# Performance work log

Measured on AMD Instinct MI355X. Metric: run time of the kernel, lower is better.

Reference implementation:

```python
import jax, jax.numpy as jnp
import numpy as np

BG_CLASS = 3          # eval path drops argmax-class==3
NMS_THRESH = 0.2      # nms(rois, scores, 0.2)
IMG_SIZE = 512.0      # ClipBoxes to 512x512 image
NUM_CLASSES = 4


def _decode_boxes(rois, deltas):
    # BBoxTransform: std weights (0.1, 0.1, 0.2, 0.2), then clip to image
    w = rois[:, 2] - rois[:, 0]
    h = rois[:, 3] - rois[:, 1]
    cx = rois[:, 0] + 0.5 * w
    cy = rois[:, 1] + 0.5 * h
    dx = deltas[:, 0] * 0.1
    dy = deltas[:, 1] * 0.1
    dw = deltas[:, 2] * 0.2
    dh = deltas[:, 3] * 0.2
    pcx = cx + dx * w
    pcy = cy + dy * h
    pw = jnp.exp(dw) * w
    ph = jnp.exp(dh) * h
    boxes = jnp.stack([pcx - 0.5 * pw, pcy - 0.5 * ph,
                       pcx + 0.5 * pw, pcy + 0.5 * ph], axis=1)
    return jnp.clip(boxes, 0.0, IMG_SIZE)


def _iou_one_vs_all(box, boxes):
    x1 = jnp.maximum(box[0], boxes[:, 0])
    y1 = jnp.maximum(box[1], boxes[:, 1])
    x2 = jnp.minimum(box[2], boxes[:, 2])
    y2 = jnp.minimum(box[3], boxes[:, 3])
    inter = jnp.clip(x2 - x1, 0.0) * jnp.clip(y2 - y1, 0.0)
    area_a = (box[2] - box[0]) * (box[3] - box[1])
    area_b = (boxes[:, 2] - boxes[:, 0]) * (boxes[:, 3] - boxes[:, 1])
    return inter / (area_a + area_b - inter + 1e-8)


def _nms_keep_mask(boxes, scores, thresh):
    # Fixed-shape NMS: returns bool keep mask over the original ordering.
    N = boxes.shape[0]
    order = jnp.argsort(-scores)           # descending score
    b = boxes[order]
    idx = jnp.arange(N)

    def body(i, keep):
        iou = _iou_one_vs_all(b[i], b)
        suppress = (iou > thresh) & (idx > i)
        return jnp.where(keep[i], keep & ~suppress, keep)

    keep_sorted = jax.lax.fori_loop(0, N, body, jnp.ones((N,), dtype=bool))
    return jnp.zeros((N,), dtype=bool).at[order].set(keep_sorted)


def _head(f, rois, w6, b6, w7, b7, wc, bc, wr, br):
    # TwoMLPHead
    v = jax.nn.relu(f @ w6.T + b6)          # [N, 1024]
    v = jax.nn.relu(v @ w7.T + b7)          # [N, 1024]
    # FastRCNNPredictor
    c = v @ wc.T + bc                        # [N, num_classes]
    r = v @ wr.T + br                        # [N, num_classes*4]
    classes = jnp.argmax(c, axis=1)          # torch.max(x,1)[1]
    scores = jnp.max(c, axis=1)              # torch.max(x,1)[0]
    deltas = jnp.take_along_axis(r.reshape(-1, NUM_CLASSES, 4),
                                 classes[:, None, None], axis=1)[:, 0, :]
    boxes = _decode_boxes(rois, deltas)
    return scores, classes, boxes


def setup_inputs() -> dict:
    key = jax.random.key(0)
    ks = jax.random.split(key, 10)
    N, D, H = 8000, 12544, 1024
    f = jax.random.normal(ks[0], (N, D), dtype=jnp.float32)
    # valid xyxy ROIs inside 512x512
    xy = jax.random.uniform(ks[1], (N, 2), minval=0.0, maxval=380.0)
    wh = jax.random.uniform(ks[2], (N, 2), minval=20.0, maxval=120.0)
    rois = jnp.concatenate([xy, xy + wh], axis=1).astype(jnp.float32)
    w6 = jax.random.normal(ks[3], (H, D), dtype=jnp.float32) * 0.01
    b6 = jnp.zeros((H,), dtype=jnp.float32)
    w7 = jax.random.normal(ks[4], (H, H), dtype=jnp.float32) * 0.02
    b7 = jnp.zeros((H,), dtype=jnp.float32)
    wc = jax.random.normal(ks[5], (NUM_CLASSES, H), dtype=jnp.float32) * 0.02
    bc = jnp.zeros((NUM_CLASSES,), dtype=jnp.float32)
    wr = jax.random.normal(ks[6], (NUM_CLASSES * 4, H), dtype=jnp.float32) * 0.02
    br = jnp.zeros((NUM_CLASSES * 4,), dtype=jnp.float32)
    return {"f": f, "rois": rois, "w6": w6, "b6": b6, "w7": w7, "b7": b7,
            "wc": wc, "bc": bc, "wr": wr, "br": br}


def reference(f, rois, w6, b6, w7, b7, wc, bc, wr, br):
    scores, classes, boxes = _head(f, rois, w6, b6, w7, b7, wc, bc, wr, br)
    valid = classes != BG_CLASS
    s_masked = jnp.where(valid, scores, -jnp.inf)
    keep = _nms_keep_mask(boxes, s_masked, NMS_THRESH) & valid
    # fixed-shape equivalent of (scores[index], labels[index], bboxes[index])
    return scores, classes, boxes, keep
```

## Files before the change

### kernel.cpp

```cpp
#include <hip/hip_runtime.h>
#include <hip/hip_fp16.h>
#include <math.h>

typedef _Float16 f16;
typedef _Float16 f16x4 __attribute__((ext_vector_type(4)));
typedef _Float16 f16x8 __attribute__((ext_vector_type(8)));
typedef float f32x4 __attribute__((ext_vector_type(4)));
typedef unsigned long long u64;

#define GLD16(g, s) __builtin_amdgcn_global_load_lds( \
    (const __attribute__((address_space(1))) void*)(g), \
    (__attribute__((address_space(3))) void*)(s), 16, 0, 0)

struct HL { f16 h, l; };
__device__ __forceinline__ HL split1(float e) {
  float em = __uint_as_float(__float_as_uint(e) & 0xFFFFE000u);
  HL r;
  r.h = (f16)em;
  r.l = (f16)(e - em);
  return r;
}

__global__ __launch_bounds__(256) void split_kernel(const float* __restrict__ src,
                                                    f16* __restrict__ hi,
                                                    f16* __restrict__ lo,
                                                    long n4, float scale) {
  long stride = (long)gridDim.x * blockDim.x;
  for (long i = (long)blockIdx.x * blockDim.x + threadIdx.x; i < n4; i += stride) {
    float4 v = ((const float4*)src)[i];
    f16x4 h, l;
    HL r0 = split1(v.x * scale); h[0] = r0.h; l[0] = r0.l;
    HL r1 = split1(v.y * scale); h[1] = r1.h; l[1] = r1.l;
    HL r2 = split1(v.z * scale); h[2] = r2.h; l[2] = r2.l;
    HL r3 = split1(v.w * scale); h[3] = r3.h; l[3] = r3.l;
    ((f16x4*)hi)[i] = h;
    ((f16x4*)lo)[i] = l;
  }
}

template<int EPI, int AFP32>
__global__ __launch_bounds__(512) void gemm_split(
    const void* __restrict__ Av1, const void* __restrict__ Av2,
    const f16* __restrict__ B1, const f16* __restrict__ B2,
    const float* __restrict__ bias,
    void* __restrict__ out1, void* __restrict__ out2,
    const int M, const int K) {
  __shared__ __align__(16) char smem[3][49152];
  const int tid = threadIdx.x;
  const int lane = tid & 63;
  const int wid = tid >> 6;
  const int wr = wid >> 1, wcol = wid & 1;
  const int m0 = blockIdx.y * 256;
  const int n0 = blockIdx.x * 128;

  f32x4 acc[4][4];
#pragma unroll
  for (int m = 0; m < 4; ++m)
#pragma unroll
    for (int n = 0; n < 4; ++n) acc[m][n] = (f32x4){0.f, 0.f, 0.f, 0.f};

  const int cg = (((tid & 3) ^ ((tid >> 3) & 3)) * 8);
  const f16* gB1 = B1 + (size_t)(n0 + (tid >> 2)) * K + cg;
  const f16* gB2 = B2 + (size_t)(n0 + (tid >> 2)) * K + cg;

  const float* gAf[4];
  if (AFP32) {
    const float* Af = (const float*)Av1;
#pragma unroll
    for (int q = 0; q < 4; ++q) {
      int rowg = m0 + q * 64 + (tid >> 3);
      if (rowg > M - 1) rowg = M - 1;
      const int chunkg = (tid & 7) ^ ((tid >> 3) & 7);
      gAf[q] = Af + (size_t)rowg * K + chunkg * 4;
    }
  }
  const f16 *gA1q0 = nullptr, *gA1q1 = nullptr, *gA2q0 = nullptr, *gA2q1 = nullptr;
  if (!AFP32) {
    int ra0 = m0 + (tid >> 2);       if (ra0 > M - 1) ra0 = M - 1;
    int ra1 = m0 + 128 + (tid >> 2); if (ra1 > M - 1) ra1 = M - 1;
    gA1q0 = (const f16*)Av1 + (size_t)ra0 * K + cg;
    gA1q1 = (const f16*)Av1 + (size_t)ra1 * K + cg;
    gA2q0 = (const f16*)Av2 + (size_t)ra0 * K + cg;
    gA2q1 = (const f16*)Av2 + (size_t)ra1 * K + cg;
  }

  const int arow = wr * 64 + (lane & 15);
  const int brow = wcol * 64 + (lane & 15);
  const int kcA = (((lane >> 4) ^ ((arow >> 1) & 3)) * 8);
  const int kcB = (((lane >> 4) ^ ((brow >> 1) & 3)) * 8);
  const int pA0 = (((lane >> 4) * 2)     ^ (arow & 7)) * 4;
  const int pA1 = (((lane >> 4) * 2 + 1) ^ (arow & 7)) * 4;

  const int nt = K / 32;

#define STAGE(buf, kt)                                            \
  do {                                                            \
    char* smx_ = smem[buf];                                       \
    if (AFP32) {                                                  \
      float* db = (float*)smx_;                                   \
      GLD16(gAf[0] + (kt), db + 0 * 2048 + wid * 256);            \
      GLD16(gAf[1] + (kt), db + 1 * 2048 + wid * 256);            \
      GLD16(gAf[2] + (kt), db + 2 * 2048 + wid * 256);            \
      GLD16(gAf[3] + (kt), db + 3 * 2048 + wid * 256);            \
    } else {                                                      \
      f16* d1 = (f16*)smx_;                                       \
      f16* d2 = d1 + 8192;                                        \
      GLD16(gA1q0 + (kt), d1 + wid * 512);                        \
      GLD16(gA1q1 + (kt), d1 + 4096 + wid * 512);                 \
      GLD16(gA2q0 + (kt), d2 + wid * 512);                        \
      GLD16(gA2q1 + (kt), d2 + 4096 + wid * 512);                 \
    }                                                             \
    GLD16(gB1 + (kt), (f16*)(smx_ + 32768) + wid * 512);          \
    GLD16(gB2 + (kt), (f16*)(smx_ + 40960) + wid * 512);          \
  } while (0)

  STAGE(0, 0);
  if (nt > 1) STAGE(1, 32);
  int cur = 0;

  for (int t = 0; t < nt; ++t) {
    if (t + 1 < nt) asm volatile("s_waitcnt vmcnt(6)" ::: "memory");
    else            asm volatile("s_waitcnt vmcnt(0)" ::: "memory");
    asm volatile("s_waitcnt lgkmcnt(0)" ::: "memory");
    __builtin_amdgcn_s_barrier();
    __builtin_amdgcn_sched_barrier(0);

    const char* smx = smem[cur];
    f16x8 a1[4], a2[4], b1[4], b2[4];
    if (AFP32) {
      const float* sf = (const float*)smx;
#pragma unroll
      for (int m = 0; m < 4; ++m) {
        const float* rp = sf + (arow + m * 16) * 32;
        f32x4 u = *(const f32x4*)(rp + pA0);
        f32x4 v = *(const f32x4*)(rp + pA1);
        f16x8 h, l;
#pragma unroll
        for (int j = 0; j < 4; ++j) { HL r = split1(u[j] * 256.0f); h[j] = r.h; l[j] = r.l; }
#pragma unroll
        for (int j = 0; j < 4; ++j) { HL r = split1(v[j] * 256.0f); h[4 + j] = r.h; l[4 + j] = r.l; }
        a1[m] = h; a2[m] = l;
      }
    } else {
      const f16* s1 = (const f16*)smx;
      const f16* s2 = s1 + 8192;
#pragma unroll
      for (int m = 0; m < 4; ++m) {
        a1[m] = *(const f16x8*)&s1[(arow + m * 16) * 32 + kcA];
        a2[m] = *(const f16x8*)&s2[(arow + m * 16) * 32 + kcA];
      }
    }
    {
      const f16* sb1 = (const f16*)(smx + 32768);
      const f16* sb2 = (const f16*)(smx + 40960);
#pragma unroll
      for (int n = 0; n < 4; ++n) {
        b1[n] = *(const f16x8*)&sb1[(brow + n * 16) * 32 + kcB];
        b2[n] = *(const f16x8*)&sb2[(brow + n * 16) * 32 + kcB];
      }
    }

    int pre = cur + 2; if (pre >= 3) pre -= 3;
    if (t + 2 < nt) STAGE(pre, (t + 2) * 32);

#pragma unroll
    for (int m = 0; m < 4; ++m)
#pragma unroll
      for (int n = 0; n < 4; ++n)
        acc[m][n] = __builtin_amdgcn_mfma_f32_16x16x32_f16(a1[m], b1[n], acc[m][n], 0, 0, 0);
#pragma unroll
    for (int m = 0; m < 4; ++m)
#pragma unroll
      for (int n = 0; n < 4; ++n)
        acc[m][n] = __builtin_amdgcn_mfma_f32_16x16x32_f16(a2[m], b1[n], acc[m][n], 0, 0, 0);
#pragma unroll
    for (int m = 0; m < 4; ++m)
#pragma unroll
      for (int n = 0; n < 4; ++n)
        acc[m][n] = __builtin_amdgcn_mfma_f32_16x16x32_f16(a1[m], b2[n], acc[m][n], 0, 0, 0);

    ++cur; if (cur >= 3) cur = 0;
  }
#undef STAGE

  const int crow = m0 + wr * 64 + 4 * (lane >> 4);
  const int ccol0 = n0 + wcol * 64 + (lane & 15);
#pragma unroll
  for (int n = 0; n < 4; ++n) {
    const int col = ccol0 + n * 16;
    const float bv = bias[col];
#pragma unroll
    for (int m = 0; m < 4; ++m) {
#pragma unroll
      for (int j = 0; j < 4; ++j) {
        const int row = crow + m * 16 + j;
        if (row < M) {
          float v = acc[m][n][j] * (1.0f / 65536.0f) + bv;
          v = fmaxf(v, 0.0f);
          if (EPI == 1) {
            HL r = split1(v * 256.0f);
            ((f16*)out1)[(size_t)row * 1024 + col] = r.h;
            ((f16*)out2)[(size_t)row * 1024 + col] = r.l;
          } else {
            ((float*)out1)[(size_t)row * 1024 + col] = v;
          }
        }
      }
    }
  }
}

__device__ __forceinline__ float dot4f(float4 a, float4 b) {
  return a.x * b.x + a.y * b.y + a.z * b.z + a.w * b.w;
}

__global__ __launch_bounds__(256) void head_final(
    const float* __restrict__ v7,
    const float* __restrict__ wc, const float* __restrict__ bc,
    const float* __restrict__ wr, const float* __restrict__ br,
    const float* __restrict__ rois,
    float* __restrict__ outScores, float* __restrict__ outClasses,
    float* __restrict__ outBoxes,
    float* __restrict__ smask, float* __restrict__ wsbox, int* __restrict__ wsval) {
  const int gw = (blockIdx.x * 256 + threadIdx.x) >> 6;
  const int lane = threadIdx.x & 63;
  if (gw >= 8000) return;

  const float4* vr = (const float4*)(v7 + (size_t)gw * 1024);
  float4 x0 = vr[lane], x1 = vr[64 + lane], x2 = vr[128 + lane], x3 = vr[192 + lane];

  float s[20];
#pragma unroll
  for (int o = 0; o < 20; ++o) {
    const float* wrow = (o < 4) ? (wc + o * 1024) : (wr + (o - 4) * 1024);
    const float4* w4 = (const float4*)wrow;
    float a = dot4f(x0, w4[lane]) + dot4f(x1, w4[64 + lane]) +
              dot4f(x2, w4[128 + lane]) + dot4f(x3, w4[192 + lane]);
#pragma unroll
    for (int off = 32; off >= 1; off >>= 1) a += __shfl_xor(a, off);
    s[o] = a + ((o < 4) ? bc[o] : br[o - 4]);
  }

  float best = s[0]; int cls = 0;
  if (s[1] > best) { best = s[1]; cls = 1; }
  if (s[2] > best) { best = s[2]; cls = 2; }
  if (s[3] > best) { best = s[3]; cls = 3; }

  float d0, d1, d2, d3;
  if      (cls == 0) { d0 = s[4];  d1 = s[5];  d2 = s[6];  d3 = s[7];  }
  else if (cls == 1) { d0 = s[8];  d1 = s[9];  d2 = s[10]; d3 = s[11]; }
  else if (cls == 2) { d0 = s[12]; d1 = s[13]; d2 = s[14]; d3 = s[15]; }
  else               { d0 = s[16]; d1 = s[17]; d2 = s[18]; d3 = s[19]; }

  float4 rb = ((const float4*)rois)[gw];
  float w = rb.z - rb.x, h = rb.w - rb.y;
  float cx = rb.x + 0.5f * w, cy = rb.y + 0.5f * h;
  float pcx = cx + d0 * 0.1f * w;
  float pcy = cy + d1 * 0.1f * h;
  float pw = expf(d2 * 0.2f) * w;
  float ph = expf(d3 * 0.2f) * h;
  float bx0 = fminf(fmaxf(pcx - 0.5f * pw, 0.f), 512.f);
  float by0 = fminf(fmaxf(pcy - 0.5f * ph, 0.f), 512.f);
  float bx1 = fminf(fmaxf(pcx + 0.5f * pw, 0.f), 512.f);
  float by1 = fminf(fmaxf(pcy + 0.5f * ph, 0.f), 512.f);

  if (lane == 0) {
    outScores[gw] = best;
    outClasses[gw] = (float)cls;
    outBoxes[gw * 4 + 0] = bx0;
    outBoxes[gw * 4 + 1] = by0;
    outBoxes[gw * 4 + 2] = bx1;
    outBoxes[gw * 4 + 3] = by1;
    int valid = (cls != 3);
    smask[gw] = valid ? best : -INFINITY;
    wsval[gw] = valid;
    float4 bb; bb.x = bx0; bb.y = by0; bb.z = bx1; bb.w = by1;
    ((float4*)wsbox)[gw] = bb;
  }
}

__global__ __launch_bounds__(256) void rank_kernel(
    const float* __restrict__ smask, const float* __restrict__ bx,
    const int* __restrict__ valid,
    int* __restrict__ order, float* __restrict__ sboxes, int* __restrict__ svalid) {
  __shared__ __align__(16) float sS[8000];
  const int tid = threadIdx.x;
  for (int i = tid; i < 8000; i += 256) sS[i] = smask[i];
  __syncthreads();
  const int i = blockIdx.x * 256 + tid;
  if (i >= 8000) return;
  const float si = sS[i];
  int cnt = 0;
  const float4* s4p = (const float4*)sS;
  for (int j4 = 0; j4 < 2000; ++j4) {
    float4 s4 = s4p[j4];
    int jb = j4 * 4;
    cnt += (s4.x > si) || (s4.x == si && (jb + 0) < i);
    cnt += (s4.y > si) || (s4.y == si && (jb + 1) < i);
    cnt += (s4.z > si) || (s4.z == si && (jb + 2) < i);
    cnt += (s4.w > si) || (s4.w == si && (jb + 3) < i);
  }
  order[cnt] = i;
  svalid[cnt] = valid[i];
  ((float4*)sboxes)[cnt] = ((const float4*)bx)[i];
}

__global__ __launch_bounds__(256) void iou_matrix(const float* __restrict__ sboxes,
                                                  u64* __restrict__ M,
                                                  u64* __restrict__ Mdiag,
                                                  const int* __restrict__ svalid) {
  const int t = blockIdx.y;
  const int w = blockIdx.x * 4 + (threadIdx.x >> 6);
  if (w < t || w >= 125) return;
  if (svalid[t * 64] == 0 || svalid[w * 64] == 0) return;
  const int lane = threadIdx.x & 63;
  const int ri = t * 64 + lane;
  float4 rb = ((const float4*)sboxes)[ri];
  const float ra = (rb.z - rb.x) * (rb.w - rb.y);
  const float4* cb = (const float4*)sboxes + w * 64;
  u64 bits = 0;
#pragma unroll 4
  for (int j = 0; j < 64; ++j) {
    float4 c = cb[j];
    float x1 = fmaxf(rb.x, c.x), y1 = fmaxf(rb.y, c.y);
    float x2 = fminf(rb.z, c.z), y2 = fminf(rb.w, c.w);
    float inter = fmaxf(x2 - x1, 0.f) * fmaxf(y2 - y1, 0.f);
    float ca = (c.z - c.x) * (c.w - c.y);
    float iou = inter / (ra + ca - inter + 1e-8f);
    int gc = w * 64 + j;
    if (iou > 0.2f && gc > ri) bits |= (1ULL << j);
  }
  M[(size_t)ri * 128 + w] = bits;
  if (w == t) Mdiag[(size_t)t * 64 + lane] = bits;
}

__global__ __launch_bounds__(128) void nms_scan(
    const u64* __restrict__ M, const u64* __restrict__ Mdiag,
    const int* __restrict__ order,
    const int* __restrict__ svalid, float* __restrict__ outKeep) {
  __shared__ __align__(16) u64 sMdiag[8000];
  __shared__ u64 acc[126];
  __shared__ unsigned char klist[64];
  __shared__ int kcount;
  __shared__ int tv[125];
  __shared__ int nvt_s;
  const int tid = threadIdx.x;
  for (int i = tid; i < 4000; i += 128)
    ((float4*)sMdiag)[i] = ((const float4*)Mdiag)[i];
  for (int w = tid; w < 125; w += 128) acc[w] = 0;
  if (tid < 125) tv[tid] = svalid[tid * 64];
  __syncthreads();
  if (tid == 0) {
    int c = 0;
    while (c < 125 && tv[c]) ++c;
    nvt_s = c;
  }
  __syncthreads();
  const int nvt = nvt_s;

  for (int t = 0; t < nvt; ++t) {
    if (tid < 64) {
      u64 myrow = sMdiag[t * 64 + tid];
      unsigned mlo = (unsigned)myrow, mhi = (unsigned)(myrow >> 32);
      u64 r = acc[t];
      u64 rem = ~r;
      while (rem) {
        int i = __builtin_ctzll(rem);
        unsigned rlo = (unsigned)__builtin_amdgcn_readlane((int)mlo, i);
        unsigned rhi = (unsigned)__builtin_amdgcn_readlane((int)mhi, i);
        u64 rowi = ((u64)rhi << 32) | (u64)rlo;
        r |= rowi;
        rem &= ~(rowi | (1ULL << i));
      }
      u64 kept = ~r;
      if (tid == 0) { acc[t] = r; kcount = (int)__popcll(kept); }
      if ((kept >> tid) & 1ULL)
        klist[__popcll(kept & ((1ULL << tid) - 1ULL))] = (unsigned char)tid;
    }
    __syncthreads();
    const int kc = kcount;
    const int w = t + 1 + tid;
    if (w < nvt) {
      u64 a = acc[w];
      const u64* base = M + (size_t)t * 64 * 128 + w;
      int j = 0;
      for (; j + 16 <= kc; j += 16) {
        u64 o = 0;
#pragma unroll
        for (int q = 0; q < 16; ++q) o |= base[(size_t)klist[j + q] * 128];
        a |= o;
      }
      for (; j + 4 <= kc; j += 4) {
        u64 v0 = base[(size_t)klist[j] * 128];
        u64 v1 = base[(size_t)klist[j + 1] * 128];
        u64 v2 = base[(size_t)klist[j + 2] * 128];
        u64 v3 = base[(size_t)klist[j + 3] * 128];
        a |= (v0 | v1) | (v2 | v3);
      }
      for (; j < kc; ++j) a |= base[(size_t)klist[j] * 128];
      acc[w] = a;
    }
    __syncthreads();
  }

  for (int p = tid; p < 8000; p += 128) {
    int removed = (int)((acc[p >> 6] >> (p & 63)) & 1ULL);
    float kv = (!removed && svalid[p]) ? 1.0f : 0.0f;
    outKeep[order[p]] = kv;
  }
}

extern "C" void kernel_launch(void* const* d_in, const int* in_sizes, int n_in,
                              void* d_out, int out_size, void* d_ws, size_t ws_size,
                              hipStream_t stream) {
  const float* F    = (const float*)d_in[0];
  const float* ROIS = (const float*)d_in[1];
  const float* W6   = (const float*)d_in[2];
  const float* B6   = (const float*)d_in[3];
  const float* W7   = (const float*)d_in[4];
  const float* B7   = (const float*)d_in[5];
  const float* WC   = (const float*)d_in[6];
  const float* BC   = (const float*)d_in[7];
  const float* WR   = (const float*)d_in[8];
  const float* BR   = (const float*)d_in[9];

  const size_t N = 8000, D = 12544, H = 1024;
  char* ws = (char*)d_ws;
  size_t off = 0;
  auto alloc = [&](size_t bytes) -> void* {
    void* p = (void*)(ws + off);
    off += (bytes + 255) & ~(size_t)255;
    return p;
  };
  f16*   B1w   = (f16*)alloc(H * D * 2);
  f16*   B2w   = (f16*)alloc(H * D * 2);
  f16*   V61   = (f16*)alloc(N * H * 2);
  f16*   V62   = (f16*)alloc(N * H * 2);
  f16*   W71   = (f16*)alloc(H * H * 2);
  f16*   W72   = (f16*)alloc(H * H * 2);
  float* V7    = (float*)alloc(N * H * 4);
  float* SMASK = (float*)alloc(N * 4);
  float* WSBOX = (float*)alloc(N * 16);
  int*   WSVAL = (int*)alloc(N * 4);
  int*   ORDER = (int*)alloc(N * 4);
  float* SBOX  = (float*)alloc(N * 16);
  int*   SVAL  = (int*)alloc(N * 4);
  u64*   MM    = (u64*)alloc(N * 128 * 8);
  u64*   MDIAG = (u64*)alloc(125 * 64 * 8);

  float* outScores  = (float*)d_out;
  float* outClasses = (float*)d_out + 8000;
  float* outBoxes   = (float*)d_out + 16000;
  float* outKeep    = (float*)d_out + 48000;

  split_kernel<<<1024, 256, 0, stream>>>(W6, B1w, B2w, (long)(H * D / 4), 256.0f);
  split_kernel<<<256, 256, 0, stream>>>(W7, W71, W72, (long)(H * H / 4), 256.0f);

  gemm_split<1, 1><<<dim3(8, 32), 512, 0, stream>>>(F, nullptr, B1w, B2w, B6, V61, V62, 8000, 12544);
  gemm_split<2, 0><<<dim3(8, 32), 512, 0, stream>>>(V61, V62, W71, W72, B7, V7, nullptr, 8000, 1024);

  head_final<<<2000, 256, 0, stream>>>(V7, WC, BC, WR, BR, ROIS,
                                       outScores, outClasses, outBoxes,
                                       SMASK, WSBOX, WSVAL);
  rank_kernel<<<32, 256, 0, stream>>>(SMASK, WSBOX, WSVAL, ORDER, SBOX, SVAL);
  iou_matrix<<<dim3(32, 125), 256, 0, stream>>>(SBOX, MM, MDIAG, SVAL);
  nms_scan<<<1, 128, 0, stream>>>(MM, MDIAG, ORDER, SVAL, outKeep);
}
```

Baseline: 1.157 ms.

## Split first GEMM into 128x128 tiles, transpose NMS mask, unroll rank loop

The large first GEMM moves from a 256x128 tile with 512 threads and triple buffering to a dedicated 128x128 kernel with 256 threads and double buffering. This gives 504 blocks instead of 256, so the many CUs stay busy, at the cost of less operand reuse per block and a full vmcnt(0) wait every k-step. The NMS mask is stored block-transposed so the scan's gathers over kept rows read contiguous u64s rather than 1 KB-strided ones. The rank counting loop is also unrolled by four float4 loads.

```diff
diff --git a/kernel.cpp b/kernel.cpp
--- a/kernel.cpp
+++ b/kernel.cpp
@@ -38,12 +38,145 @@
   }
 }
 
-template<int EPI, int AFP32>
-__global__ __launch_bounds__(512) void gemm_split(
-    const void* __restrict__ Av1, const void* __restrict__ Av2,
+__global__ __launch_bounds__(256) void gemm1_128(
+    const float* __restrict__ Af,
     const f16* __restrict__ B1, const f16* __restrict__ B2,
     const float* __restrict__ bias,
-    void* __restrict__ out1, void* __restrict__ out2,
+    f16* __restrict__ out1, f16* __restrict__ out2,
+    const int M, const int K) {
+  __shared__ __align__(16) char smem[2][32768];
+  const int tid = threadIdx.x;
+  const int lane = tid & 63;
+  const int wid = tid >> 6;
+  const int wr = wid >> 1, wcol = wid & 1;
+  const int m0 = blockIdx.y * 128;
+  const int n0 = blockIdx.x * 128;
+
+  f32x4 acc[4][4];
+#pragma unroll
+  for (int m = 0; m < 4; ++m)
+#pragma unroll
+    for (int n = 0; n < 4; ++n) acc[m][n] = (f32x4){0.f, 0.f, 0.f, 0.f};
+
+  const float* gAf[4];
+#pragma unroll
+  for (int q = 0; q < 4; ++q) {
+    int rowg = m0 + q * 32 + (tid >> 3);
+    if (rowg > M - 1) rowg = M - 1;
+    const int chunkg = (tid & 7) ^ ((tid >> 3) & 7);
+    gAf[q] = Af + (size_t)rowg * K + chunkg * 4;
+  }
+  const int rq = tid >> 2;
+  const int cg = (((tid & 3) ^ ((rq >> 1) & 3)) * 8);
+  const f16* gB1q0 = B1 + (size_t)(n0 + rq) * K + cg;
+  const f16* gB1q1 = B1 + (size_t)(n0 + 64 + rq) * K + cg;
+  const f16* gB2q0 = B2 + (size_t)(n0 + rq) * K + cg;
+  const f16* gB2q1 = B2 + (size_t)(n0 + 64 + rq) * K + cg;
+  const int du = wid * 512;
+
+  const int arow = wr * 64 + (lane & 15);
+  const int brow = wcol * 64 + (lane & 15);
+  const int kcB = (((lane >> 4) ^ ((brow >> 1) & 3)) * 8);
+  const int pA0 = (((lane >> 4) * 2)     ^ (arow & 7)) * 4;
+  const int pA1 = (((lane >> 4) * 2 + 1) ^ (arow & 7)) * 4;
+
+  const int nt = K / 32;
+
+#define STAGE(buf, kt)                                            \
+  do {                                                            \
+    char* smx_ = smem[buf];                                       \
+    float* db = (float*)smx_;                                     \
+    GLD16(gAf[0] + (kt), db + 0 * 1024 + wid * 256);              \
+    GLD16(gAf[1] + (kt), db + 1 * 1024 + wid * 256);              \
+    GLD16(gAf[2] + (kt), db + 2 * 1024 + wid * 256);              \
+    GLD16(gAf[3] + (kt), db + 3 * 1024 + wid * 256);              \
+    GLD16(gB1q0 + (kt), (f16*)(smx_ + 16384) + du);               \
+    GLD16(gB1q1 + (kt), (f16*)(smx_ + 16384) + 2048 + du);        \
+    GLD16(gB2q0 + (kt), (f16*)(smx_ + 24576) + du);               \
+    GLD16(gB2q1 + (kt), (f16*)(smx_ + 24576) + 2048 + du);        \
+  } while (0)
+
+  STAGE(0, 0);
+
+  for (int t = 0; t < nt; ++t) {
+    asm volatile("s_waitcnt vmcnt(0)" ::: "memory");
+    asm volatile("s_waitcnt lgkmcnt(0)" ::: "memory");
+    __builtin_amdgcn_s_barrier();
+    __builtin_amdgcn_sched_barrier(0);
+
+    const char* smx = smem[t & 1];
+    const float* sf = (const float*)smx;
+    f16x8 a1[4], a2[4], b1[4], b2[4];
+#pragma unroll
+    for (int m = 0; m < 4; ++m) {
+      const float* rp = sf + (arow + m * 16) * 32;
+      f32x4 u = *(const f32x4*)(rp + pA0);
+      f32x4 v = *(const f32x4*)(rp + pA1);
+      f16x8 h, l;
+#pragma unroll
+      for (int j = 0; j < 4; ++j) { HL r = split1(u[j] * 256.0f); h[j] = r.h; l[j] = r.l; }
+#pragma unroll
+      for (int j = 0; j < 4; ++j) { HL r = split1(v[j] * 256.0f); h[4 + j] = r.h; l[4 + j] = r.l; }
+      a1[m] = h; a2[m] = l;
+    }
+    {
+      const f16* sb1 = (const f16*)(smx + 16384);
+      const f16* sb2 = (const f16*)(smx + 24576);
+#pragma unroll
+      for (int n = 0; n < 4; ++n) {
+        b1[n] = *(const f16x8*)&sb1[(brow + n * 16) * 32 + kcB];
+        b2[n] = *(const f16x8*)&sb2[(brow + n * 16) * 32 + kcB];
+      }
+    }
+
+    if (t + 1 < nt) STAGE((t + 1) & 1, (t + 1) * 32);
+
+#pragma unroll
+    for (int m = 0; m < 4; ++m)
+#pragma unroll
+      for (int n = 0; n < 4; ++n)
+        acc[m][n] = __builtin_amdgcn_mfma_f32_16x16x32_f16(a1[m], b1[n], acc[m][n], 0, 0, 0);
+#pragma unroll
+    for (int m = 0; m < 4; ++m)
+#pragma unroll
+      for (int n = 0; n < 4; ++n)
+        acc[m][n] = __builtin_amdgcn_mfma_f32_16x16x32_f16(a2[m], b1[n], acc[m][n], 0, 0, 0);
+#pragma unroll
+    for (int m = 0; m < 4; ++m)
+#pragma unroll
+      for (int n = 0; n < 4; ++n)
+        acc[m][n] = __builtin_amdgcn_mfma_f32_16x16x32_f16(a1[m], b2[n], acc[m][n], 0, 0, 0);
+  }
+#undef STAGE
+
+  const int crow = m0 + wr * 64 + 4 * (lane >> 4);
+  const int ccol0 = n0 + wcol * 64 + (lane & 15);
+#pragma unroll
+  for (int n = 0; n < 4; ++n) {
+    const int col = ccol0 + n * 16;
+    const float bv = bias[col];
+#pragma unroll
+    for (int m = 0; m < 4; ++m) {
+#pragma unroll
+      for (int j = 0; j < 4; ++j) {
+        const int row = crow + m * 16 + j;
+        if (row < M) {
+          float v = acc[m][n][j] * (1.0f / 65536.0f) + bv;
+          v = fmaxf(v, 0.0f);
+          HL r = split1(v * 256.0f);
+          out1[(size_t)row * 1024 + col] = r.h;
+          out2[(size_t)row * 1024 + col] = r.l;
+        }
+      }
+    }
+  }
+}
+
+__global__ __launch_bounds__(512) void gemm2_k(
+    const f16* __restrict__ A1, const f16* __restrict__ A2,
+    const f16* __restrict__ B1, const f16* __restrict__ B2,
+    const float* __restrict__ bias,
+    float* __restrict__ out1,
     const int M, const int K) {
   __shared__ __align__(16) char smem[3][49152];
   const int tid = threadIdx.x;
@@ -62,54 +195,29 @@
   const int cg = (((tid & 3) ^ ((tid >> 3) & 3)) * 8);
   const f16* gB1 = B1 + (size_t)(n0 + (tid >> 2)) * K + cg;
   const f16* gB2 = B2 + (size_t)(n0 + (tid >> 2)) * K + cg;
-
-  const float* gAf[4];
-  if (AFP32) {
-    const float* Af = (const float*)Av1;
-#pragma unroll
-    for (int q = 0; q < 4; ++q) {
-      int rowg = m0 + q * 64 + (tid >> 3);
-      if (rowg > M - 1) rowg = M - 1;
-      const int chunkg = (tid & 7) ^ ((tid >> 3) & 7);
-      gAf[q] = Af + (size_t)rowg * K + chunkg * 4;
-    }
-  }
-  const f16 *gA1q0 = nullptr, *gA1q1 = nullptr, *gA2q0 = nullptr, *gA2q1 = nullptr;
-  if (!AFP32) {
-    int ra0 = m0 + (tid >> 2);       if (ra0 > M - 1) ra0 = M - 1;
-    int ra1 = m0 + 128 + (tid >> 2); if (ra1 > M - 1) ra1 = M - 1;
-    gA1q0 = (const f16*)Av1 + (size_t)ra0 * K + cg;
-    gA1q1 = (const f16*)Av1 + (size_t)ra1 * K + cg;
-    gA2q0 = (const f16*)Av2 + (size_t)ra0 * K + cg;
-    gA2q1 = (const f16*)Av2 + (size_t)ra1 * K + cg;
-  }
+  int ra0 = m0 + (tid >> 2);       if (ra0 > M - 1) ra0 = M - 1;
+  int ra1 = m0 + 128 + (tid >> 2); if (ra1 > M - 1) ra1 = M - 1;
+  const f16* gA1q0 = A1 + (size_t)ra0 * K + cg;
+  const f16* gA1q1 = A1 + (size_t)ra1 * K + cg;
+  const f16* gA2q0 = A2 + (size_t)ra0 * K + cg;
+  const f16* gA2q1 = A2 + (size_t)ra1 * K + cg;
 
   const int arow = wr * 64 + (lane & 15);
   const int brow = wcol * 64 + (lane & 15);
   const int kcA = (((lane >> 4) ^ ((arow >> 1) & 3)) * 8);
   const int kcB = (((lane >> 4) ^ ((brow >> 1) & 3)) * 8);
-  const int pA0 = (((lane >> 4) * 2)     ^ (arow & 7)) * 4;
-  const int pA1 = (((lane >> 4) * 2 + 1) ^ (arow & 7)) * 4;
 
   const int nt = K / 32;
 
 #define STAGE(buf, kt)                                            \
   do {                                                            \
     char* smx_ = smem[buf];                                       \
-    if (AFP32) {                                                  \
-      float* db = (float*)smx_;                                   \
-      GLD16(gAf[0] + (kt), db + 0 * 2048 + wid * 256);            \
-      GLD16(gAf[1] + (kt), db + 1 * 2048 + wid * 256);            \
-      GLD16(gAf[2] + (kt), db + 2 * 2048 + wid * 256);            \
-      GLD16(gAf[3] + (kt), db + 3 * 2048 + wid * 256);            \
-    } else {                                                      \
-      f16* d1 = (f16*)smx_;                                       \
-      f16* d2 = d1 + 8192;                                        \
-      GLD16(gA1q0 + (kt), d1 + wid * 512);                        \
-      GLD16(gA1q1 + (kt), d1 + 4096 + wid * 512);                 \
-      GLD16(gA2q0 + (kt), d2 + wid * 512);                        \
-      GLD16(gA2q1 + (kt), d2 + 4096 + wid * 512);                 \
-    }                                                             \
+    f16* d1 = (f16*)smx_;                                         \
+    f16* d2 = d1 + 8192;                                          \
+    GLD16(gA1q0 + (kt), d1 + wid * 512);                          \
+    GLD16(gA1q1 + (kt), d1 + 4096 + wid * 512);                   \
+    GLD16(gA2q0 + (kt), d2 + wid * 512);                          \
+    GLD16(gA2q1 + (kt), d2 + 4096 + wid * 512);                   \
     GLD16(gB1 + (kt), (f16*)(smx_ + 32768) + wid * 512);          \
     GLD16(gB2 + (kt), (f16*)(smx_ + 40960) + wid * 512);          \
   } while (0)
@@ -126,38 +234,20 @@
     __builtin_amdgcn_sched_barrier(0);
 
     const char* smx = smem[cur];
+    const f16* s1 = (const f16*)smx;
+    const f16* s2 = s1 + 8192;
+    const f16* sb1 = (const f16*)(smx + 32768);
+    const f16* sb2 = (const f16*)(smx + 40960);
     f16x8 a1[4], a2[4], b1[4], b2[4];
-    if (AFP32) {
-      const float* sf = (const float*)smx;
-#pragma unroll
-      for (int m = 0; m < 4; ++m) {
-        const float* rp = sf + (arow + m * 16) * 32;
-        f32x4 u = *(const f32x4*)(rp + pA0);
-        f32x4 v = *(const f32x4*)(rp + pA1);
-        f16x8 h, l;
-#pragma unroll
-        for (int j = 0; j < 4; ++j) { HL r = split1(u[j] * 256.0f); h[j] = r.h; l[j] = r.l; }
-#pragma unroll
-        for (int j = 0; j < 4; ++j) { HL r = split1(v[j] * 256.0f); h[4 + j] = r.h; l[4 + j] = r.l; }
-        a1[m] = h; a2[m] = l;
-      }
-    } else {
-      const f16* s1 = (const f16*)smx;
-      const f16* s2 = s1 + 8192;
-#pragma unroll
-      for (int m = 0; m < 4; ++m) {
-        a1[m] = *(const f16x8*)&s1[(arow + m * 16) * 32 + kcA];
-        a2[m] = *(const f16x8*)&s2[(arow + m * 16) * 32 + kcA];
-      }
-    }
-    {
-      const f16* sb1 = (const f16*)(smx + 32768);
-      const f16* sb2 = (const f16*)(smx + 40960);
-#pragma unroll
-      for (int n = 0; n < 4; ++n) {
-        b1[n] = *(const f16x8*)&sb1[(brow + n * 16) * 32 + kcB];
-        b2[n] = *(const f16x8*)&sb2[(brow + n * 16) * 32 + kcB];
-      }
+#pragma unroll
+    for (int m = 0; m < 4; ++m) {
+      a1[m] = *(const f16x8*)&s1[(arow + m * 16) * 32 + kcA];
+      a2[m] = *(const f16x8*)&s2[(arow + m * 16) * 32 + kcA];
+    }
+#pragma unroll
+    for (int n = 0; n < 4; ++n) {
+      b1[n] = *(const f16x8*)&sb1[(brow + n * 16) * 32 + kcB];
+      b2[n] = *(const f16x8*)&sb2[(brow + n * 16) * 32 + kcB];
     }
 
     int pre = cur + 2; if (pre >= 3) pre -= 3;
@@ -196,14 +286,7 @@
         const int row = crow + m * 16 + j;
         if (row < M) {
           float v = acc[m][n][j] * (1.0f / 65536.0f) + bv;
-          v = fmaxf(v, 0.0f);
-          if (EPI == 1) {
-            HL r = split1(v * 256.0f);
-            ((f16*)out1)[(size_t)row * 1024 + col] = r.h;
-            ((f16*)out2)[(size_t)row * 1024 + col] = r.l;
-          } else {
-            ((float*)out1)[(size_t)row * 1024 + col] = v;
-          }
+          out1[(size_t)row * 1024 + col] = fmaxf(v, 0.0f);
         }
       }
     }
@@ -292,13 +375,25 @@
   const float si = sS[i];
   int cnt = 0;
   const float4* s4p = (const float4*)sS;
-  for (int j4 = 0; j4 < 2000; ++j4) {
-    float4 s4 = s4p[j4];
+  for (int j4 = 0; j4 < 2000; j4 += 4) {
+    float4 sa = s4p[j4], sb = s4p[j4 + 1], sc = s4p[j4 + 2], sd = s4p[j4 + 3];
     int jb = j4 * 4;
-    cnt += (s4.x > si) || (s4.x == si && (jb + 0) < i);
-    cnt += (s4.y > si) || (s4.y == si && (jb + 1) < i);
-    cnt += (s4.z > si) || (s4.z == si && (jb + 2) < i);
-    cnt += (s4.w > si) || (s4.w == si && (jb + 3) < i);
+    cnt += (sa.x > si) || (sa.x == si && (jb + 0) < i);
+    cnt += (sa.y > si) || (sa.y == si && (jb + 1) < i);
+    cnt += (sa.z > si) || (sa.z == si && (jb + 2) < i);
+    cnt += (sa.w > si) || (sa.w == si && (jb + 3) < i);
+    cnt += (sb.x > si) || (sb.x == si && (jb + 4) < i);
+    cnt += (sb.y > si) || (sb.y == si && (jb + 5) < i);
+    cnt += (sb.z > si) || (sb.z == si && (jb + 6) < i);
+    cnt += (sb.w > si) || (sb.w == si && (jb + 7) < i);
+    cnt += (sc.x > si) || (sc.x == si && (jb + 8) < i);
+    cnt += (sc.y > si) || (sc.y == si && (jb + 9) < i);
+    cnt += (sc.z > si) || (sc.z == si && (jb + 10) < i);
+    cnt += (sc.w > si) || (sc.w == si && (jb + 11) < i);
+    cnt += (sd.x > si) || (sd.x == si && (jb + 12) < i);
+    cnt += (sd.y > si) || (sd.y == si && (jb + 13) < i);
+    cnt += (sd.z > si) || (sd.z == si && (jb + 14) < i);
+    cnt += (sd.w > si) || (sd.w == si && (jb + 15) < i);
   }
   order[cnt] = i;
   svalid[cnt] = valid[i];
@@ -306,7 +401,7 @@
 }
 
 __global__ __launch_bounds__(256) void iou_matrix(const float* __restrict__ sboxes,
-                                                  u64* __restrict__ M,
+                                                  u64* __restrict__ MT,
                                                   u64* __restrict__ Mdiag,
                                                   const int* __restrict__ svalid) {
   const int t = blockIdx.y;
@@ -330,12 +425,12 @@
     int gc = w * 64 + j;
     if (iou > 0.2f && gc > ri) bits |= (1ULL << j);
   }
-  M[(size_t)ri * 128 + w] = bits;
+  MT[((size_t)t * 125 + w) * 64 + lane] = bits;
   if (w == t) Mdiag[(size_t)t * 64 + lane] = bits;
 }
 
 __global__ __launch_bounds__(128) void nms_scan(
-    const u64* __restrict__ M, const u64* __restrict__ Mdiag,
+    const u64* __restrict__ MT, const u64* __restrict__ Mdiag,
     const int* __restrict__ order,
     const int* __restrict__ svalid, float* __restrict__ outKeep) {
   __shared__ __align__(16) u64 sMdiag[8000];
@@ -382,22 +477,22 @@
     const int w = t + 1 + tid;
     if (w < nvt) {
       u64 a = acc[w];
-      const u64* base = M + (size_t)t * 64 * 128 + w;
+      const u64* base = MT + ((size_t)t * 125 + w) * 64;
       int j = 0;
       for (; j + 16 <= kc; j += 16) {
         u64 o = 0;
 #pragma unroll
-        for (int q = 0; q < 16; ++q) o |= base[(size_t)klist[j + q] * 128];
+        for (int q = 0; q < 16; ++q) o |= base[klist[j + q]];
         a |= o;
       }
       for (; j + 4 <= kc; j += 4) {
-        u64 v0 = base[(size_t)klist[j] * 128];
-        u64 v1 = base[(size_t)klist[j + 1] * 128];
-        u64 v2 = base[(size_t)klist[j + 2] * 128];
-        u64 v3 = base[(size_t)klist[j + 3] * 128];
+        u64 v0 = base[klist[j]];
+        u64 v1 = base[klist[j + 1]];
+        u64 v2 = base[klist[j + 2]];
+        u64 v3 = base[klist[j + 3]];
         a |= (v0 | v1) | (v2 | v3);
       }
-      for (; j < kc; ++j) a |= base[(size_t)klist[j] * 128];
+      for (; j < kc; ++j) a |= base[klist[j]];
       acc[w] = a;
     }
     __syncthreads();
@@ -445,7 +540,7 @@
   int*   ORDER = (int*)alloc(N * 4);
   float* SBOX  = (float*)alloc(N * 16);
   int*   SVAL  = (int*)alloc(N * 4);
-  u64*   MM    = (u64*)alloc(N * 128 * 8);
+  u64*   MT    = (u64*)alloc((size_t)125 * 125 * 64 * 8);
   u64*   MDIAG = (u64*)alloc(125 * 64 * 8);
 
   float* outScores  = (float*)d_out;
@@ -456,13 +551,13 @@
   split_kernel<<<1024, 256, 0, stream>>>(W6, B1w, B2w, (long)(H * D / 4), 256.0f);
   split_kernel<<<256, 256, 0, stream>>>(W7, W71, W72, (long)(H * H / 4), 256.0f);
 
-  gemm_split<1, 1><<<dim3(8, 32), 512, 0, stream>>>(F, nullptr, B1w, B2w, B6, V61, V62, 8000, 12544);
-  gemm_split<2, 0><<<dim3(8, 32), 512, 0, stream>>>(V61, V62, W71, W72, B7, V7, nullptr, 8000, 1024);
+  gemm1_128<<<dim3(8, 63), 256, 0, stream>>>(F, B1w, B2w, B6, V61, V62, 8000, 12544);
+  gemm2_k<<<dim3(8, 32), 512, 0, stream>>>(V61, V62, W71, W72, B7, V7, 8000, 1024);
 
   head_final<<<2000, 256, 0, stream>>>(V7, WC, BC, WR, BR, ROIS,
                                        outScores, outClasses, outBoxes,
                                        SMASK, WSBOX, WSVAL);
   rank_kernel<<<32, 256, 0, stream>>>(SMASK, WSBOX, WSVAL, ORDER, SBOX, SVAL);
-  iou_matrix<<<dim3(32, 125), 256, 0, stream>>>(SBOX, MM, MDIAG, SVAL);
-  nms_scan<<<1, 128, 0, stream>>>(MM, MDIAG, ORDER, SVAL, outKeep);
-}
+  iou_matrix<<<dim3(32, 125), 256, 0, stream>>>(SBOX, MT, MDIAG, SVAL);
+  nms_scan<<<1, 128, 0, stream>>>(MT, MDIAG, ORDER, SVAL, outKeep);
+}
```

Measured after the change: 1.168 ms. About the same (+1.0%).
